# Optimization experiments

Measured on AMD Instinct MI355X. Metric: run time of the kernel, lower is better.

## Reference

```python
import jax, jax.numpy as jnp
import numpy as np

N = 50000
E = 800000
IN_C = 256
HID = 256
OUT_C = 64
HEADS = 4
NEG_SLOPE = 0.2  # PyG GATConv default leaky_relu slope


def gat_conv(x, edge_index, W, a_src, a_dst, bias, heads, concat):
    """PyG-style GATConv (add_self_loops=True, eval mode so no dropout).
    x: [N, F_in]; W: [F_in, heads*C]; a_src/a_dst: [heads, C]; bias: [heads*C] or [C].
    """
    n = x.shape[0]
    # add self loops
    loops = jnp.arange(n, dtype=edge_index.dtype)
    src = jnp.concatenate([edge_index[0], loops])
    dst = jnp.concatenate([edge_index[1], loops])
    h = (x @ W).reshape(n, heads, -1)               # [N, H, C]
    alpha_src = jnp.einsum('nhc,hc->nh', h, a_src)  # [N, H]
    alpha_dst = jnp.einsum('nhc,hc->nh', h, a_dst)
    e = jax.nn.leaky_relu(alpha_src[src] + alpha_dst[dst], NEG_SLOPE)  # [E', H]
    # segment softmax over incoming edges of each dst node
    m = jax.ops.segment_max(e, dst, num_segments=n)        # [N, H]
    w = jnp.exp(e - m[dst])
    denom = jax.ops.segment_sum(w, dst, num_segments=n)    # [N, H]
    att = w / (denom[dst] + 1e-16)                          # [E', H]
    out = jax.ops.segment_sum(h[src] * att[:, :, None], dst, num_segments=n)  # [N, H, C]
    out = out.reshape(n, -1) if concat else out.mean(axis=1)
    return out + bias


def setup_inputs() -> dict:
    key = jax.random.key(0)
    ks = jax.random.split(key, 10)
    c1 = HID // HEADS  # per-head channels of layer 1
    s_in = 1.0 / np.sqrt(IN_C)
    s_hid = 1.0 / np.sqrt(HID)
    return {
        'x': jax.random.normal(ks[0], (N, IN_C), dtype=jnp.float32),
        'edge_index': jax.random.randint(ks[1], (2, E), 0, N, dtype=jnp.int64),
        'W1': jax.random.normal(ks[2], (IN_C, HEADS * c1), dtype=jnp.float32) * s_in,
        'a_src1': jax.random.normal(ks[3], (HEADS, c1), dtype=jnp.float32) * s_in,
        'a_dst1': jax.random.normal(ks[4], (HEADS, c1), dtype=jnp.float32) * s_in,
        'b1': jnp.zeros((HEADS * c1,), dtype=jnp.float32),
        'W2': jax.random.normal(ks[5], (HID, OUT_C), dtype=jnp.float32) * s_hid,
        'a_src2': jax.random.normal(ks[6], (1, OUT_C), dtype=jnp.float32) * s_hid,
        'a_dst2': jax.random.normal(ks[7], (1, OUT_C), dtype=jnp.float32) * s_hid,
        'b2': jnp.zeros((OUT_C,), dtype=jnp.float32),
    }


def reference(x, edge_index, W1, a_src1, a_dst1, b1, W2, a_src2, a_dst2, b2):
    h = gat_conv(x, edge_index, W1, a_src1, a_dst1, b1, heads=HEADS, concat=True)
    h = jax.nn.elu(h)
    # dropout: eval mode -> identity
    return gat_conv(h, edge_index, W2, a_src2, a_dst2, b2, heads=1, concat=False)
```

## Files before the change

### kernel.cpp

```cpp
#include <hip/hip_runtime.h>
#include <math.h>

#define NN 50000
#define NE 800000
#define ET (NE + NN)
#define FIN 256
#define HIDC 256
#define OC 64
#define NH 4
#define NEG 0.2f
#define CAP 64
#define NSTRIPES (NN / 16)

typedef __attribute__((ext_vector_type(8))) short bf16x8;
typedef __attribute__((ext_vector_type(4))) float f32x4;

__device__ __forceinline__ unsigned short f2bf(float f) {
    unsigned u = __float_as_uint(f);
    unsigned r = (u + 0x7FFFu + ((u >> 16) & 1u)) >> 16;
    return (unsigned short)r;
}
__device__ __forceinline__ float bflo(unsigned v) { return __uint_as_float(v << 16); }
__device__ __forceinline__ float bfhi(unsigned v) { return __uint_as_float(v & 0xffff0000u); }

__global__ void k_scatter(const int* __restrict__ ei, int* __restrict__ cnt,
                          int* __restrict__ esrc) {
    int e = blockIdx.x * blockDim.x + threadIdx.x;
    if (e >= ET) return;
    int s, d;
    if (e < NE) { s = ei[e]; d = ei[NE + e]; } else { s = d = e - NE; }
    int k = atomicAdd(&cnt[d], 1);
    if (k < CAP) esrc[(size_t)d * CAP + k] = s;
}

__global__ void k_pack(const float* __restrict__ W, unsigned short* __restrict__ Bp,
                       int N, int NTL, int total) {
    int t = blockIdx.x * 256 + threadIdx.x;
    if (t >= total) return;
    int lane = t & 63;
    int ntl = (t >> 6) % NTL;
    int ks = ((t >> 6) / NTL) & 7;
    int hy = t / (64 * NTL * 8);
    int col = hy * NTL * 16 + ntl * 16 + (lane & 15);
    int k0 = ks * 32 + (lane >> 4) * 8;
#pragma unroll
    for (int i = 0; i < 8; i++) Bp[(size_t)t * 8 + i] = f2bf(W[(k0 + i) * N + col]);
}

template <int NTL, bool F32A, int NHEADS>
__global__ void __launch_bounds__(256) k_gemm(const void* __restrict__ Av,
                                              const unsigned short* __restrict__ Bp,
                                              unsigned short* __restrict__ D, int N,
                                              const float* __restrict__ aS,
                                              const float* __restrict__ aD,
                                              float* __restrict__ asOut,
                                              float* __restrict__ adOut) {
    constexpr int TOT = 8 * NTL * 64 * 8;
    constexpr int HPH = (NTL * 16) / 64;
    __shared__ unsigned short lds[TOT];
    const unsigned short* src = Bp + (size_t)blockIdx.y * TOT;
    for (int i = threadIdx.x * 8; i < TOT; i += 256 * 8)
        *(uint4*)&lds[i] = *(const uint4*)&src[i];
    __syncthreads();
    int wave = threadIdx.x >> 6, lane = threadIdx.x & 63;
    int l15 = lane & 15, lh = lane >> 4;
    int coloff = blockIdx.y * NTL * 16;
    float aSv[NTL], aDv[NTL];
#pragma unroll
    for (int nt = 0; nt < NTL; nt++) {
        aSv[nt] = aS[coloff + nt * 16 + l15];
        aDv[nt] = aD[coloff + nt * 16 + l15];
    }
    for (int st = blockIdx.x * 4 + wave; st < NSTRIPES; st += gridDim.x * 4) {
        f32x4 acc[NTL];
#pragma unroll
        for (int t = 0; t < NTL; t++) acc[t] = (f32x4){0.f, 0.f, 0.f, 0.f};
#pragma unroll
        for (int ks = 0; ks < 8; ks++) {
            bf16x8 a;
            if (F32A) {
                const float* arow = (const float*)Av + (size_t)(st * 16 + l15) * 256 + lh * 8 + ks * 32;
                float4 fa = *(const float4*)arow;
                float4 fb = *(const float4*)(arow + 4);
                a[0] = (short)f2bf(fa.x); a[1] = (short)f2bf(fa.y);
                a[2] = (short)f2bf(fa.z); a[3] = (short)f2bf(fa.w);
                a[4] = (short)f2bf(fb.x); a[5] = (short)f2bf(fb.y);
                a[6] = (short)f2bf(fb.z); a[7] = (short)f2bf(fb.w);
            } else {
                a = *(const bf16x8*)((const unsigned short*)Av + (size_t)(st * 16 + l15) * 256 + lh * 8 + ks * 32);
            }
#pragma unroll
            for (int nt = 0; nt < NTL; nt++) {
                bf16x8 b = *(const bf16x8*)&lds[((size_t)(ks * NTL + nt) * 64 + lane) * 8];
                acc[nt] = __builtin_amdgcn_mfma_f32_16x16x32_bf16(a, b, acc[nt], 0, 0, 0);
            }
        }
        unsigned short* dbase = D + (size_t)st * 16 * N + coloff;
#pragma unroll
        for (int nt = 0; nt < NTL; nt++)
#pragma unroll
            for (int r = 0; r < 4; r++)
                dbase[(lh * 4 + r) * N + nt * 16 + l15] = f2bf(acc[nt][r]);
#pragma unroll
        for (int r = 0; r < 4; r++) {
#pragma unroll
            for (int g = 0; g < HPH; g++) {
                float ps = 0.f, pd = 0.f;
#pragma unroll
                for (int q = 0; q < 4; q++) {
                    int nt = g * 4 + q;
                    ps += acc[nt][r] * aSv[nt];
                    pd += acc[nt][r] * aDv[nt];
                }
#pragma unroll
                for (int off = 1; off < 16; off <<= 1) {
                    ps += __shfl_xor(ps, off);
                    pd += __shfl_xor(pd, off);
                }
                if (l15 == 0) {
                    int row = st * 16 + lh * 4 + r;
                    int hidx = blockIdx.y * HPH + g;
                    asOut[row * NHEADS + hidx] = ps;
                    adOut[row * NHEADS + hidx] = pd;
                }
            }
        }
    }
}


__global__ void k_agg1f(const int* __restrict__ cnt, const int* __restrict__ esrc,
                        const unsigned short* __restrict__ h, const float* __restrict__ as,
                        const float* __restrict__ ad, const float* __restrict__ bias,
                        unsigned short* __restrict__ out) {
    __shared__ float wlds[4][64][4];
    int wave = threadIdx.x >> 6;
    int n = blockIdx.x * 4 + wave;
    int lane = threadIdx.x & 63;
    if (n >= NN) return;
    int deg = cnt[n];
    deg = deg < CAP ? deg : CAP;
    const int* bucket = &esrc[(size_t)n * CAP];
    bool act = lane < deg;
    int myS = act ? bucket[lane] : 0;
    float4 adv = *(const float4*)&ad[n * NH];
    float e0 = -INFINITY, e1 = -INFINITY, e2 = -INFINITY, e3 = -INFINITY;
    if (act) {
        float4 av = *(const float4*)&as[myS * NH];
        e0 = av.x + adv.x; e0 = e0 > 0.f ? e0 : NEG * e0;
        e1 = av.y + adv.y; e1 = e1 > 0.f ? e1 : NEG * e1;
        e2 = av.z + adv.z; e2 = e2 > 0.f ? e2 : NEG * e2;
        e3 = av.w + adv.w; e3 = e3 > 0.f ? e3 : NEG * e3;
    }
    float m0 = e0, m1 = e1, m2 = e2, m3 = e3;
    for (int off = 32; off; off >>= 1) {
        m0 = fmaxf(m0, __shfl_xor(m0, off));
        m1 = fmaxf(m1, __shfl_xor(m1, off));
        m2 = fmaxf(m2, __shfl_xor(m2, off));
        m3 = fmaxf(m3, __shfl_xor(m3, off));
    }
    float w0 = act ? expf(e0 - m0) : 0.f;
    float w1 = act ? expf(e1 - m1) : 0.f;
    float w2 = act ? expf(e2 - m2) : 0.f;
    float w3 = act ? expf(e3 - m3) : 0.f;
    *(float4*)&wlds[wave][lane][0] = (float4){w0, w1, w2, w3};
    float s0 = w0, s1 = w1, s2 = w2, s3 = w3;
    for (int off = 32; off; off >>= 1) {
        s0 += __shfl_xor(s0, off);
        s1 += __shfl_xor(s1, off);
        s2 += __shfl_xor(s2, off);
        s3 += __shfl_xor(s3, off);
    }
    int hh = lane >> 4;
    int cbase = hh * 64 + (lane & 15) * 4;
    float ssel = hh == 0 ? s0 : hh == 1 ? s1 : hh == 2 ? s2 : s3;
    float rsel = 1.f / (ssel + 1e-16f);
    const float* wcol = &wlds[wave][0][hh];
    const unsigned short* hb = h + cbase;
    float acc0 = 0.f, acc1 = 0.f, acc2 = 0.f, acc3 = 0.f;
    int degP = (deg + 3) & ~3;
    for (int j = 0; j < degP; j += 4) {
#pragma unroll
        for (int u = 0; u < 4; u++) {
            int s = __shfl(myS, j + u);
            float w = wcol[(j + u) * 4];
            uint2 pv = *(const uint2*)&hb[(size_t)s * HIDC];
            acc0 += w * bflo(pv.x);
            acc1 += w * bfhi(pv.x);
            acc2 += w * bflo(pv.y);
            acc3 += w * bfhi(pv.y);
        }
    }
    float4 bv = *(const float4*)&bias[cbase];
    float v0 = acc0 * rsel + bv.x; v0 = v0 > 0.f ? v0 : expm1f(v0);
    float v1 = acc1 * rsel + bv.y; v1 = v1 > 0.f ? v1 : expm1f(v1);
    float v2 = acc2 * rsel + bv.z; v2 = v2 > 0.f ? v2 : expm1f(v2);
    float v3 = acc3 * rsel + bv.w; v3 = v3 > 0.f ? v3 : expm1f(v3);
    uint2 ov;
    ov.x = (unsigned)f2bf(v0) | ((unsigned)f2bf(v1) << 16);
    ov.y = (unsigned)f2bf(v2) | ((unsigned)f2bf(v3) << 16);
    *(uint2*)&out[(size_t)n * HIDC + cbase] = ov;
}

__global__ void k_agg2f(const int* __restrict__ cnt, const int* __restrict__ esrc,
                        const unsigned short* __restrict__ h, const float* __restrict__ as,
                        const float* __restrict__ ad, const float* __restrict__ bias,
                        float* __restrict__ out) {
    __shared__ float wlds[4][64];
    int wave = threadIdx.x >> 6;
    int n = blockIdx.x * 4 + wave;
    int lane = threadIdx.x & 63;
    if (n >= NN) return;
    int deg = cnt[n];
    deg = deg < CAP ? deg : CAP;
    const int* bucket = &esrc[(size_t)n * CAP];
    bool act = lane < deg;
    int myS = act ? bucket[lane] : 0;
    float adv = ad[n];
    float e = -INFINITY;
    if (act) {
        e = as[myS] + adv;
        e = e > 0.f ? e : NEG * e;
    }
    float m = e;
    for (int off = 32; off; off >>= 1) m = fmaxf(m, __shfl_xor(m, off));
    float w = act ? expf(e - m) : 0.f;
    wlds[wave][lane] = w;
    float s = w;
    for (int off = 32; off; off >>= 1) s += __shfl_xor(s, off);
    float rd = 1.f / (s + 1e-16f);

    int sub = lane >> 4;
    int cw = (lane & 15) * 4;
    const unsigned short* hb = h + cw;
    float acc0 = 0.f, acc1 = 0.f, acc2 = 0.f, acc3 = 0.f;
    int degP = (deg + 3) & ~3;
    for (int j = 0; j < degP; j += 4) {
        int jj = j + sub;
        int sj = __shfl(myS, jj);
        float wj = wlds[wave][jj];
        uint2 pv = *(const uint2*)&hb[(size_t)sj * OC];
        acc0 += wj * bflo(pv.x);
        acc1 += wj * bfhi(pv.x);
        acc2 += wj * bflo(pv.y);
        acc3 += wj * bfhi(pv.y);
    }
#pragma unroll
    for (int off = 16; off < 64; off <<= 1) {
        acc0 += __shfl_xor(acc0, off);
        acc1 += __shfl_xor(acc1, off);
        acc2 += __shfl_xor(acc2, off);
        acc3 += __shfl_xor(acc3, off);
    }
    if (lane < 16) {
        float4 bv = *(const float4*)&bias[cw];
        float4 o;
        o.x = acc0 * rd + bv.x;
        o.y = acc1 * rd + bv.y;
        o.z = acc2 * rd + bv.z;
        o.w = acc3 * rd + bv.w;
        *(float4*)&out[(size_t)n * OC + cw] = o;
    }
}

extern "C" void kernel_launch(void* const* d_in, const int* in_sizes, int n_in,
                              void* d_out, int out_size, void* d_ws, size_t ws_size,
                              hipStream_t stream) {
    const float* x   = (const float*)d_in[0];
    const int*   ei  = (const int*)d_in[1];
    const float* W1  = (const float*)d_in[2];
    const float* aS1 = (const float*)d_in[3];
    const float* aD1 = (const float*)d_in[4];
    const float* b1  = (const float*)d_in[5];
    const float* W2  = (const float*)d_in[6];
    const float* aS2 = (const float*)d_in[7];
    const float* aD2 = (const float*)d_in[8];
    const float* b2  = (const float*)d_in[9];
    float* out = (float*)d_out;

    char* p = (char*)d_ws;
    auto alloc = [&](size_t nbytes) {
        char* r = p;
        p += (nbytes + 255) & ~(size_t)255;
        return r;
    };
    unsigned short* h1b   = (unsigned short*)alloc((size_t)NN * HIDC * 2);
    unsigned short* act1b = (unsigned short*)alloc((size_t)NN * HIDC * 2);
    unsigned short* h2b   = (unsigned short*)alloc((size_t)NN * OC * 2);
    unsigned short* Bp1   = (unsigned short*)alloc((size_t)2 * 8 * 8 * 64 * 8 * 2);
    unsigned short* Bp2   = (unsigned short*)alloc((size_t)1 * 8 * 4 * 64 * 8 * 2);
    float* as1  = (float*)alloc((size_t)NN * NH * 4);
    float* ad1  = (float*)alloc((size_t)NN * NH * 4);
    float* as2  = (float*)alloc((size_t)NN * 4);
    float* ad2  = (float*)alloc((size_t)NN * 4);
    int*   cnt  = (int*)alloc((size_t)NN * 4);
    int*   esrc = (int*)alloc((size_t)NN * CAP * 4);

    hipMemsetAsync(cnt, 0, (size_t)NN * 4, stream);

    k_scatter<<<(ET + 255) / 256, 256, 0, stream>>>(ei, cnt, esrc);
    k_pack<<<(2 * 8 * 8 * 64 + 255) / 256, 256, 0, stream>>>(W1, Bp1, HIDC, 8, 2 * 8 * 8 * 64);
    k_pack<<<(1 * 8 * 4 * 64 + 255) / 256, 256, 0, stream>>>(W2, Bp2, OC, 4, 1 * 8 * 4 * 64);

    k_gemm<8, true, NH><<<dim3(256, 2), 256, 0, stream>>>(x, Bp1, h1b, HIDC, aS1, aD1, as1, ad1);
    k_agg1f<<<(NN + 3) / 4, 256, 0, stream>>>(cnt, esrc, h1b, as1, ad1, b1, act1b);

    k_gemm<4, false, 1><<<dim3(512, 1), 256, 0, stream>>>(act1b, Bp2, h2b, OC, aS2, aD2, as2, ad2);
    k_agg2f<<<(NN + 3) / 4, 256, 0, stream>>>(cnt, esrc, h2b, as2, ad2, b2, out);
}
```

Measured before the change: 224.9 us.

## Pre-convert x to bf16, double-stripe GEMM, widen agg1 gathers with split edges

Adds a kernel converting x to bf16 before the first GEMM, removing in-loop f32-to-bf16 conversion. The GEMM now computes two 16-row stripes per wave so each LDS B fragment feeds two MFMAs, with grid sizes adjusted. The layer-1 aggregation uses 16-byte gathers per lane, with wave halves processing alternate edges and combining via a cross-half shuffle. The extra conversion pass adds a full read and write of x, which may offset the GEMM savings.

```diff
diff --git a/kernel.cpp b/kernel.cpp
--- a/kernel.cpp
+++ b/kernel.cpp
@@ -11,6 +11,7 @@
 #define NEG 0.2f
 #define CAP 64
 #define NSTRIPES (NN / 16)
+#define NGROUPS ((NSTRIPES + 1) / 2)
 
 typedef __attribute__((ext_vector_type(8))) short bf16x8;
 typedef __attribute__((ext_vector_type(4))) float f32x4;
@@ -31,6 +32,20 @@
     if (e < NE) { s = ei[e]; d = ei[NE + e]; } else { s = d = e - NE; }
     int k = atomicAdd(&cnt[d], 1);
     if (k < CAP) esrc[(size_t)d * CAP + k] = s;
+}
+
+__global__ void k_cvt(const float* __restrict__ x, unsigned short* __restrict__ xb,
+                      int n) {
+    int i = (blockIdx.x * 256 + threadIdx.x) * 8;
+    if (i >= n) return;
+    float4 f0 = *(const float4*)&x[i];
+    float4 f1 = *(const float4*)&x[i + 4];
+    uint4 o;
+    o.x = (unsigned)f2bf(f0.x) | ((unsigned)f2bf(f0.y) << 16);
+    o.y = (unsigned)f2bf(f0.z) | ((unsigned)f2bf(f0.w) << 16);
+    o.z = (unsigned)f2bf(f1.x) | ((unsigned)f2bf(f1.y) << 16);
+    o.w = (unsigned)f2bf(f1.z) | ((unsigned)f2bf(f1.w) << 16);
+    *(uint4*)&xb[i] = o;
 }
 
 __global__ void k_pack(const float* __restrict__ W, unsigned short* __restrict__ Bp,
@@ -47,8 +62,8 @@
     for (int i = 0; i < 8; i++) Bp[(size_t)t * 8 + i] = f2bf(W[(k0 + i) * N + col]);
 }
 
-template <int NTL, bool F32A, int NHEADS>
-__global__ void __launch_bounds__(256) k_gemm(const void* __restrict__ Av,
+template <int NTL, int NHEADS>
+__global__ void __launch_bounds__(256) k_gemm(const unsigned short* __restrict__ A,
                                               const unsigned short* __restrict__ Bp,
                                               unsigned short* __restrict__ D, int N,
                                               const float* __restrict__ aS,
@@ -71,57 +86,58 @@
         aSv[nt] = aS[coloff + nt * 16 + l15];
         aDv[nt] = aD[coloff + nt * 16 + l15];
     }
-    for (int st = blockIdx.x * 4 + wave; st < NSTRIPES; st += gridDim.x * 4) {
-        f32x4 acc[NTL];
-#pragma unroll
-        for (int t = 0; t < NTL; t++) acc[t] = (f32x4){0.f, 0.f, 0.f, 0.f};
+    for (int g = blockIdx.x * 4 + wave; g < NGROUPS; g += gridDim.x * 4) {
+        int st0 = g * 2;
+        bool two = (st0 + 1 < NSTRIPES);
+        const unsigned short* arow0 = A + (size_t)(st0 * 16 + l15) * 256 + lh * 8;
+        const unsigned short* arow1 = two ? arow0 + 16 * 256 : arow0;
+        f32x4 acc[2][NTL];
+#pragma unroll
+        for (int m = 0; m < 2; m++)
+#pragma unroll
+            for (int t = 0; t < NTL; t++) acc[m][t] = (f32x4){0.f, 0.f, 0.f, 0.f};
 #pragma unroll
         for (int ks = 0; ks < 8; ks++) {
-            bf16x8 a;
-            if (F32A) {
-                const float* arow = (const float*)Av + (size_t)(st * 16 + l15) * 256 + lh * 8 + ks * 32;
-                float4 fa = *(const float4*)arow;
-                float4 fb = *(const float4*)(arow + 4);
-                a[0] = (short)f2bf(fa.x); a[1] = (short)f2bf(fa.y);
-                a[2] = (short)f2bf(fa.z); a[3] = (short)f2bf(fa.w);
-                a[4] = (short)f2bf(fb.x); a[5] = (short)f2bf(fb.y);
-                a[6] = (short)f2bf(fb.z); a[7] = (short)f2bf(fb.w);
-            } else {
-                a = *(const bf16x8*)((const unsigned short*)Av + (size_t)(st * 16 + l15) * 256 + lh * 8 + ks * 32);
-            }
+            bf16x8 a0 = *(const bf16x8*)(arow0 + ks * 32);
+            bf16x8 a1 = *(const bf16x8*)(arow1 + ks * 32);
 #pragma unroll
             for (int nt = 0; nt < NTL; nt++) {
                 bf16x8 b = *(const bf16x8*)&lds[((size_t)(ks * NTL + nt) * 64 + lane) * 8];
-                acc[nt] = __builtin_amdgcn_mfma_f32_16x16x32_bf16(a, b, acc[nt], 0, 0, 0);
+                acc[0][nt] = __builtin_amdgcn_mfma_f32_16x16x32_bf16(a0, b, acc[0][nt], 0, 0, 0);
+                acc[1][nt] = __builtin_amdgcn_mfma_f32_16x16x32_bf16(a1, b, acc[1][nt], 0, 0, 0);
             }
         }
-        unsigned short* dbase = D + (size_t)st * 16 * N + coloff;
-#pragma unroll
-        for (int nt = 0; nt < NTL; nt++)
-#pragma unroll
-            for (int r = 0; r < 4; r++)
-                dbase[(lh * 4 + r) * N + nt * 16 + l15] = f2bf(acc[nt][r]);
-#pragma unroll
-        for (int r = 0; r < 4; r++) {
-#pragma unroll
-            for (int g = 0; g < HPH; g++) {
-                float ps = 0.f, pd = 0.f;
-#pragma unroll
-                for (int q = 0; q < 4; q++) {
-                    int nt = g * 4 + q;
-                    ps += acc[nt][r] * aSv[nt];
-                    pd += acc[nt][r] * aDv[nt];
-                }
-#pragma unroll
-                for (int off = 1; off < 16; off <<= 1) {
-                    ps += __shfl_xor(ps, off);
-                    pd += __shfl_xor(pd, off);
-                }
-                if (l15 == 0) {
-                    int row = st * 16 + lh * 4 + r;
-                    int hidx = blockIdx.y * HPH + g;
-                    asOut[row * NHEADS + hidx] = ps;
-                    adOut[row * NHEADS + hidx] = pd;
+        int nm = two ? 2 : 1;
+        for (int m = 0; m < nm; m++) {
+            int strow = (st0 + m) * 16;
+            unsigned short* dbase = D + (size_t)strow * N + coloff;
+#pragma unroll
+            for (int nt = 0; nt < NTL; nt++)
+#pragma unroll
+                for (int r = 0; r < 4; r++)
+                    dbase[(lh * 4 + r) * N + nt * 16 + l15] = f2bf(acc[m][nt][r]);
+#pragma unroll
+            for (int r = 0; r < 4; r++) {
+#pragma unroll
+                for (int gg = 0; gg < HPH; gg++) {
+                    float ps = 0.f, pd = 0.f;
+#pragma unroll
+                    for (int q = 0; q < 4; q++) {
+                        int nt = gg * 4 + q;
+                        ps += acc[m][nt][r] * aSv[nt];
+                        pd += acc[m][nt][r] * aDv[nt];
+                    }
+#pragma unroll
+                    for (int off = 1; off < 16; off <<= 1) {
+                        ps += __shfl_xor(ps, off);
+                        pd += __shfl_xor(pd, off);
+                    }
+                    if (l15 == 0) {
+                        int row = strow + lh * 4 + r;
+                        int hidx = blockIdx.y * HPH + gg;
+                        asOut[row * NHEADS + hidx] = ps;
+                        adOut[row * NHEADS + hidx] = pd;
+                    }
                 }
             }
         }
@@ -171,35 +187,56 @@
         s2 += __shfl_xor(s2, off);
         s3 += __shfl_xor(s3, off);
     }
-    int hh = lane >> 4;
-    int cbase = hh * 64 + (lane & 15) * 4;
-    float ssel = hh == 0 ? s0 : hh == 1 ? s1 : hh == 2 ? s2 : s3;
-    float rsel = 1.f / (ssel + 1e-16f);
+    int sub = lane >> 5;
+    int l31 = lane & 31;
+    int hh = l31 >> 3;
+    int c8 = l31 * 8;
+    float rsel = 1.f / ((hh == 0 ? s0 : hh == 1 ? s1 : hh == 2 ? s2 : s3) + 1e-16f);
+    const unsigned short* hb = h + c8;
+    float a0 = 0.f, a1 = 0.f, a2 = 0.f, a3 = 0.f, a4 = 0.f, a5 = 0.f, a6 = 0.f, a7 = 0.f;
+    int degP = (deg + 1) & ~1;
     const float* wcol = &wlds[wave][0][hh];
-    const unsigned short* hb = h + cbase;
-    float acc0 = 0.f, acc1 = 0.f, acc2 = 0.f, acc3 = 0.f;
-    int degP = (deg + 3) & ~3;
-    for (int j = 0; j < degP; j += 4) {
-#pragma unroll
-        for (int u = 0; u < 4; u++) {
-            int s = __shfl(myS, j + u);
-            float w = wcol[(j + u) * 4];
-            uint2 pv = *(const uint2*)&hb[(size_t)s * HIDC];
-            acc0 += w * bflo(pv.x);
-            acc1 += w * bfhi(pv.x);
-            acc2 += w * bflo(pv.y);
-            acc3 += w * bfhi(pv.y);
-        }
-    }
-    float4 bv = *(const float4*)&bias[cbase];
-    float v0 = acc0 * rsel + bv.x; v0 = v0 > 0.f ? v0 : expm1f(v0);
-    float v1 = acc1 * rsel + bv.y; v1 = v1 > 0.f ? v1 : expm1f(v1);
-    float v2 = acc2 * rsel + bv.z; v2 = v2 > 0.f ? v2 : expm1f(v2);
-    float v3 = acc3 * rsel + bv.w; v3 = v3 > 0.f ? v3 : expm1f(v3);
-    uint2 ov;
-    ov.x = (unsigned)f2bf(v0) | ((unsigned)f2bf(v1) << 16);
-    ov.y = (unsigned)f2bf(v2) | ((unsigned)f2bf(v3) << 16);
-    *(uint2*)&out[(size_t)n * HIDC + cbase] = ov;
+#pragma unroll 2
+    for (int j = 0; j < degP; j += 2) {
+        int jj = j + sub;
+        int sj = __shfl(myS, jj);
+        float wj = wcol[jj * 4];
+        uint4 pv = *(const uint4*)&hb[(size_t)sj * HIDC];
+        a0 += wj * bflo(pv.x);
+        a1 += wj * bfhi(pv.x);
+        a2 += wj * bflo(pv.y);
+        a3 += wj * bfhi(pv.y);
+        a4 += wj * bflo(pv.z);
+        a5 += wj * bfhi(pv.z);
+        a6 += wj * bflo(pv.w);
+        a7 += wj * bfhi(pv.w);
+    }
+    a0 += __shfl_xor(a0, 32);
+    a1 += __shfl_xor(a1, 32);
+    a2 += __shfl_xor(a2, 32);
+    a3 += __shfl_xor(a3, 32);
+    a4 += __shfl_xor(a4, 32);
+    a5 += __shfl_xor(a5, 32);
+    a6 += __shfl_xor(a6, 32);
+    a7 += __shfl_xor(a7, 32);
+    if (sub == 0) {
+        float4 bv0 = *(const float4*)&bias[c8];
+        float4 bv1 = *(const float4*)&bias[c8 + 4];
+        float v0 = a0 * rsel + bv0.x; v0 = v0 > 0.f ? v0 : expm1f(v0);
+        float v1 = a1 * rsel + bv0.y; v1 = v1 > 0.f ? v1 : expm1f(v1);
+        float v2 = a2 * rsel + bv0.z; v2 = v2 > 0.f ? v2 : expm1f(v2);
+        float v3 = a3 * rsel + bv0.w; v3 = v3 > 0.f ? v3 : expm1f(v3);
+        float v4 = a4 * rsel + bv1.x; v4 = v4 > 0.f ? v4 : expm1f(v4);
+        float v5 = a5 * rsel + bv1.y; v5 = v5 > 0.f ? v5 : expm1f(v5);
+        float v6 = a6 * rsel + bv1.z; v6 = v6 > 0.f ? v6 : expm1f(v6);
+        float v7 = a7 * rsel + bv1.w; v7 = v7 > 0.f ? v7 : expm1f(v7);
+        uint4 ov;
+        ov.x = (unsigned)f2bf(v0) | ((unsigned)f2bf(v1) << 16);
+        ov.y = (unsigned)f2bf(v2) | ((unsigned)f2bf(v3) << 16);
+        ov.z = (unsigned)f2bf(v4) | ((unsigned)f2bf(v5) << 16);
+        ov.w = (unsigned)f2bf(v6) | ((unsigned)f2bf(v7) << 16);
+        *(uint4*)&out[(size_t)n * HIDC + c8] = ov;
+    }
 }
 
 __global__ void k_agg2f(const int* __restrict__ cnt, const int* __restrict__ esrc,
@@ -284,6 +321,7 @@
         p += (nbytes + 255) & ~(size_t)255;
         return r;
     };
+    unsigned short* xb    = (unsigned short*)alloc((size_t)NN * FIN * 2);
     unsigned short* h1b   = (unsigned short*)alloc((size_t)NN * HIDC * 2);
     unsigned short* act1b = (unsigned short*)alloc((size_t)NN * HIDC * 2);
     unsigned short* h2b   = (unsigned short*)alloc((size_t)NN * OC * 2);
@@ -299,12 +337,13 @@
     hipMemsetAsync(cnt, 0, (size_t)NN * 4, stream);
 
     k_scatter<<<(ET + 255) / 256, 256, 0, stream>>>(ei, cnt, esrc);
+    k_cvt<<<(NN * FIN / 8 + 255) / 256, 256, 0, stream>>>(x, xb, NN * FIN);
     k_pack<<<(2 * 8 * 8 * 64 + 255) / 256, 256, 0, stream>>>(W1, Bp1, HIDC, 8, 2 * 8 * 8 * 64);
     k_pack<<<(1 * 8 * 4 * 64 + 255) / 256, 256, 0, stream>>>(W2, Bp2, OC, 4, 1 * 8 * 4 * 64);
 
-    k_gemm<8, true, NH><<<dim3(256, 2), 256, 0, stream>>>(x, Bp1, h1b, HIDC, aS1, aD1, as1, ad1);
+    k_gemm<8, NH><<<dim3(196, 2), 256, 0, stream>>>(xb, Bp1, h1b, HIDC, aS1, aD1, as1, ad1);
     k_agg1f<<<(NN + 3) / 4, 256, 0, stream>>>(cnt, esrc, h1b, as1, ad1, b1, act1b);
 
-    k_gemm<4, false, 1><<<dim3(512, 1), 256, 0, stream>>>(act1b, Bp2, h2b, OC, aS2, aD2, as2, ad2);
+    k_gemm<4, 1><<<dim3(392, 1), 256, 0, stream>>>(act1b, Bp2, h2b, OC, aS2, aD2, as2, ad2);
     k_agg2f<<<(NN + 3) / 4, 256, 0, stream>>>(cnt, esrc, h2b, as2, ad2, b2, out);
 }
```

New measurement: 237.3 us. 1.05x slower.

## Pre-convert x to bf16, process two row stripes per wave, use 16-bit edge indices

Applied to the files above, without the earlier changes.

Adds a kernel that converts x to bf16 ahead of time, so the first GEMM reads bf16 A instead of converting fp32 inside the loop. Each wave now handles two 16-row stripes, preloading all A fragments and reusing every LDS B fragment for two MFMAs. The grid is resized to match. Edge source indices are stored as unsigned short, halving bucket traffic; node ids up to 50000 fit, but this depends on N staying below 65536.

```diff
diff --git a/kernel.cpp b/kernel.cpp
--- a/kernel.cpp
+++ b/kernel.cpp
@@ -11,6 +11,7 @@
 #define NEG 0.2f
 #define CAP 64
 #define NSTRIPES (NN / 16)
+#define NGROUPS ((NSTRIPES + 1) / 2)
 
 typedef __attribute__((ext_vector_type(8))) short bf16x8;
 typedef __attribute__((ext_vector_type(4))) float f32x4;
@@ -24,13 +25,27 @@
 __device__ __forceinline__ float bfhi(unsigned v) { return __uint_as_float(v & 0xffff0000u); }
 
 __global__ void k_scatter(const int* __restrict__ ei, int* __restrict__ cnt,
-                          int* __restrict__ esrc) {
+                          unsigned short* __restrict__ esrc) {
     int e = blockIdx.x * blockDim.x + threadIdx.x;
     if (e >= ET) return;
     int s, d;
     if (e < NE) { s = ei[e]; d = ei[NE + e]; } else { s = d = e - NE; }
     int k = atomicAdd(&cnt[d], 1);
-    if (k < CAP) esrc[(size_t)d * CAP + k] = s;
+    if (k < CAP) esrc[(size_t)d * CAP + k] = (unsigned short)s;
+}
+
+__global__ void k_cvt(const float* __restrict__ x, unsigned short* __restrict__ xb,
+                      int n) {
+    int i = (blockIdx.x * 256 + threadIdx.x) * 8;
+    if (i >= n) return;
+    float4 f0 = *(const float4*)&x[i];
+    float4 f1 = *(const float4*)&x[i + 4];
+    uint4 o;
+    o.x = (unsigned)f2bf(f0.x) | ((unsigned)f2bf(f0.y) << 16);
+    o.y = (unsigned)f2bf(f0.z) | ((unsigned)f2bf(f0.w) << 16);
+    o.z = (unsigned)f2bf(f1.x) | ((unsigned)f2bf(f1.y) << 16);
+    o.w = (unsigned)f2bf(f1.z) | ((unsigned)f2bf(f1.w) << 16);
+    *(uint4*)&xb[i] = o;
 }
 
 __global__ void k_pack(const float* __restrict__ W, unsigned short* __restrict__ Bp,
@@ -47,8 +62,8 @@
     for (int i = 0; i < 8; i++) Bp[(size_t)t * 8 + i] = f2bf(W[(k0 + i) * N + col]);
 }
 
-template <int NTL, bool F32A, int NHEADS>
-__global__ void __launch_bounds__(256) k_gemm(const void* __restrict__ Av,
+template <int NTL, int NHEADS>
+__global__ void __launch_bounds__(256) k_gemm(const unsigned short* __restrict__ A,
                                               const unsigned short* __restrict__ Bp,
                                               unsigned short* __restrict__ D, int N,
                                               const float* __restrict__ aS,
@@ -71,57 +86,61 @@
         aSv[nt] = aS[coloff + nt * 16 + l15];
         aDv[nt] = aD[coloff + nt * 16 + l15];
     }
-    for (int st = blockIdx.x * 4 + wave; st < NSTRIPES; st += gridDim.x * 4) {
-        f32x4 acc[NTL];
-#pragma unroll
-        for (int t = 0; t < NTL; t++) acc[t] = (f32x4){0.f, 0.f, 0.f, 0.f};
+    for (int g = blockIdx.x * 4 + wave; g < NGROUPS; g += gridDim.x * 4) {
+        int st0 = g * 2;
+        bool two = (st0 + 1 < NSTRIPES);
+        const unsigned short* arow0 = A + (size_t)(st0 * 16 + l15) * 256 + lh * 8;
+        const unsigned short* arow1 = two ? arow0 + 16 * 256 : arow0;
+        bf16x8 a0[8], a1[8];
+#pragma unroll
+        for (int ks = 0; ks < 8; ks++) a0[ks] = *(const bf16x8*)(arow0 + ks * 32);
+#pragma unroll
+        for (int ks = 0; ks < 8; ks++) a1[ks] = *(const bf16x8*)(arow1 + ks * 32);
+        f32x4 acc[2][NTL];
+#pragma unroll
+        for (int m = 0; m < 2; m++)
+#pragma unroll
+            for (int t = 0; t < NTL; t++) acc[m][t] = (f32x4){0.f, 0.f, 0.f, 0.f};
 #pragma unroll
         for (int ks = 0; ks < 8; ks++) {
-            bf16x8 a;
-            if (F32A) {
-                const float* arow = (const float*)Av + (size_t)(st * 16 + l15) * 256 + lh * 8 + ks * 32;
-                float4 fa = *(const float4*)arow;
-                float4 fb = *(const float4*)(arow + 4);
-                a[0] = (short)f2bf(fa.x); a[1] = (short)f2bf(fa.y);
-                a[2] = (short)f2bf(fa.z); a[3] = (short)f2bf(fa.w);
-                a[4] = (short)f2bf(fb.x); a[5] = (short)f2bf(fb.y);
-                a[6] = (short)f2bf(fb.z); a[7] = (short)f2bf(fb.w);
-            } else {
-                a = *(const bf16x8*)((const unsigned short*)Av + (size_t)(st * 16 + l15) * 256 + lh * 8 + ks * 32);
-            }
 #pragma unroll
             for (int nt = 0; nt < NTL; nt++) {
                 bf16x8 b = *(const bf16x8*)&lds[((size_t)(ks * NTL + nt) * 64 + lane) * 8];
-                acc[nt] = __builtin_amdgcn_mfma_f32_16x16x32_bf16(a, b, acc[nt], 0, 0, 0);
+                acc[0][nt] = __builtin_amdgcn_mfma_f32_16x16x32_bf16(a0[ks], b, acc[0][nt], 0, 0, 0);
+                acc[1][nt] = __builtin_amdgcn_mfma_f32_16x16x32_bf16(a1[ks], b, acc[1][nt], 0, 0, 0);
             }
         }
-        unsigned short* dbase = D + (size_t)st * 16 * N + coloff;
-#pragma unroll
-        for (int nt = 0; nt < NTL; nt++)
-#pragma unroll
-            for (int r = 0; r < 4; r++)
-                dbase[(lh * 4 + r) * N + nt * 16 + l15] = f2bf(acc[nt][r]);
-#pragma unroll
-        for (int r = 0; r < 4; r++) {
-#pragma unroll
-            for (int g = 0; g < HPH; g++) {
-                float ps = 0.f, pd = 0.f;
-#pragma unroll
-                for (int q = 0; q < 4; q++) {
-                    int nt = g * 4 + q;
-                    ps += acc[nt][r] * aSv[nt];
-                    pd += acc[nt][r] * aDv[nt];
-                }
-#pragma unroll
-                for (int off = 1; off < 16; off <<= 1) {
-                    ps += __shfl_xor(ps, off);
-                    pd += __shfl_xor(pd, off);
-                }
-                if (l15 == 0) {
-                    int row = st * 16 + lh * 4 + r;
-                    int hidx = blockIdx.y * HPH + g;
-                    asOut[row * NHEADS + hidx] = ps;
-                    adOut[row * NHEADS + hidx] = pd;
+        int nm = two ? 2 : 1;
+        for (int m = 0; m < nm; m++) {
+            int strow = (st0 + m) * 16;
+            unsigned short* dbase = D + (size_t)strow * N + coloff;
+#pragma unroll
+            for (int nt = 0; nt < NTL; nt++)
+#pragma unroll
+                for (int r = 0; r < 4; r++)
+                    dbase[(lh * 4 + r) * N + nt * 16 + l15] = f2bf(acc[m][nt][r]);
+#pragma unroll
+            for (int r = 0; r < 4; r++) {
+#pragma unroll
+                for (int gg = 0; gg < HPH; gg++) {
+                    float ps = 0.f, pd = 0.f;
+#pragma unroll
+                    for (int q = 0; q < 4; q++) {
+                        int nt = gg * 4 + q;
+                        ps += acc[m][nt][r] * aSv[nt];
+                        pd += acc[m][nt][r] * aDv[nt];
+                    }
+#pragma unroll
+                    for (int off = 1; off < 16; off <<= 1) {
+                        ps += __shfl_xor(ps, off);
+                        pd += __shfl_xor(pd, off);
+                    }
+                    if (l15 == 0) {
+                        int row = strow + lh * 4 + r;
+                        int hidx = blockIdx.y * HPH + gg;
+                        asOut[row * NHEADS + hidx] = ps;
+                        adOut[row * NHEADS + hidx] = pd;
+                    }
                 }
             }
         }
@@ -129,7 +148,7 @@
 }
 
 
-__global__ void k_agg1f(const int* __restrict__ cnt, const int* __restrict__ esrc,
+__global__ void k_agg1f(const int* __restrict__ cnt, const unsigned short* __restrict__ esrc,
                         const unsigned short* __restrict__ h, const float* __restrict__ as,
                         const float* __restrict__ ad, const float* __restrict__ bias,
                         unsigned short* __restrict__ out) {
@@ -140,9 +159,9 @@
     if (n >= NN) return;
     int deg = cnt[n];
     deg = deg < CAP ? deg : CAP;
-    const int* bucket = &esrc[(size_t)n * CAP];
+    const unsigned short* bucket = &esrc[(size_t)n * CAP];
     bool act = lane < deg;
-    int myS = act ? bucket[lane] : 0;
+    int myS = act ? (int)bucket[lane] : 0;
     float4 adv = *(const float4*)&ad[n * NH];
     float e0 = -INFINITY, e1 = -INFINITY, e2 = -INFINITY, e3 = -INFINITY;
     if (act) {
@@ -202,7 +221,7 @@
     *(uint2*)&out[(size_t)n * HIDC + cbase] = ov;
 }
 
-__global__ void k_agg2f(const int* __restrict__ cnt, const int* __restrict__ esrc,
+__global__ void k_agg2f(const int* __restrict__ cnt, const unsigned short* __restrict__ esrc,
                         const unsigned short* __restrict__ h, const float* __restrict__ as,
                         const float* __restrict__ ad, const float* __restrict__ bias,
                         float* __restrict__ out) {
@@ -213,9 +232,9 @@
     if (n >= NN) return;
     int deg = cnt[n];
     deg = deg < CAP ? deg : CAP;
-    const int* bucket = &esrc[(size_t)n * CAP];
+    const unsigned short* bucket = &esrc[(size_t)n * CAP];
     bool act = lane < deg;
-    int myS = act ? bucket[lane] : 0;
+    int myS = act ? (int)bucket[lane] : 0;
     float adv = ad[n];
     float e = -INFINITY;
     if (act) {
@@ -284,6 +303,7 @@
         p += (nbytes + 255) & ~(size_t)255;
         return r;
     };
+    unsigned short* xb    = (unsigned short*)alloc((size_t)NN * FIN * 2);
     unsigned short* h1b   = (unsigned short*)alloc((size_t)NN * HIDC * 2);
     unsigned short* act1b = (unsigned short*)alloc((size_t)NN * HIDC * 2);
     unsigned short* h2b   = (unsigned short*)alloc((size_t)NN * OC * 2);
@@ -294,17 +314,18 @@
     float* as2  = (float*)alloc((size_t)NN * 4);
     float* ad2  = (float*)alloc((size_t)NN * 4);
     int*   cnt  = (int*)alloc((size_t)NN * 4);
-    int*   esrc = (int*)alloc((size_t)NN * CAP * 4);
+    unsigned short* esrc = (unsigned short*)alloc((size_t)NN * CAP * 2);
 
     hipMemsetAsync(cnt, 0, (size_t)NN * 4, stream);
 
     k_scatter<<<(ET + 255) / 256, 256, 0, stream>>>(ei, cnt, esrc);
+    k_cvt<<<(NN * FIN / 8 + 255) / 256, 256, 0, stream>>>(x, xb, NN * FIN);
     k_pack<<<(2 * 8 * 8 * 64 + 255) / 256, 256, 0, stream>>>(W1, Bp1, HIDC, 8, 2 * 8 * 8 * 64);
     k_pack<<<(1 * 8 * 4 * 64 + 255) / 256, 256, 0, stream>>>(W2, Bp2, OC, 4, 1 * 8 * 4 * 64);
 
-    k_gemm<8, true, NH><<<dim3(256, 2), 256, 0, stream>>>(x, Bp1, h1b, HIDC, aS1, aD1, as1, ad1);
+    k_gemm<8, NH><<<dim3(196, 2), 256, 0, stream>>>(xb, Bp1, h1b, HIDC, aS1, aD1, as1, ad1);
     k_agg1f<<<(NN + 3) / 4, 256, 0, stream>>>(cnt, esrc, h1b, as1, ad1, b1, act1b);
 
-    k_gemm<4, false, 1><<<dim3(512, 1), 256, 0, stream>>>(act1b, Bp2, h2b, OC, aS2, aD2, as2, ad2);
+    k_gemm<4, 1><<<dim3(196, 1), 256, 0, stream>>>(act1b, Bp2, h2b, OC, aS2, aD2, as2, ad2);
     k_agg2f<<<(NN + 3) / 4, 256, 0, stream>>>(cnt, esrc, h2b, as2, ad2, b2, out);
 }
```

Result: no change. 228.7 us (+1.7%).
